# Optimization experiments

Measured on AMD Instinct MI355X. Metric: run time of the kernel, lower is better.

The kernel has to match this reference:

```python
import jax, jax.numpy as jnp
import numpy as np

NUM_JOINT_LIST = [8, 10, 12, 14, 16, 18, 20, 22, 24, 9, 13, 17]
NUM_GLOBAL_LIST = [1, 0, 1, 1, 0, 1, 1, 1, 0, 1, 1, 1]
M = len(NUM_JOINT_LIST)
B, T, JMAX = 16, 128, 24
H, HEADS, L, RANK = 256, 8, 4, 8
DH = H // HEADS
LAYERSCALE = 1e-4


def setup_inputs():
    key = jax.random.key(0)
    ks = jax.random.split(key, 40)
    m_idx = jax.random.randint(ks[0], (B,), 0, M)
    nj = jnp.array(NUM_JOINT_LIST)[m_idx]
    valid = jnp.arange(JMAX)[None, :] < nj[:, None]  # (B, J) real joints of each morphology
    jtype = jax.random.randint(ks[1], (B, JMAX), 0, 3)  # 0 slide, 1 hinge, 2 global
    has_g = (jnp.array(NUM_GLOBAL_LIST) > 0)[m_idx][:, None]
    jtype = jnp.where((jtype == 2) & ~has_g, 0, jtype)
    tile = lambda m: jnp.broadcast_to(m[:, None, :], (B, T, JMAX))
    slide_mask = tile((jtype == 0) & valid)
    hinge_mask = tile((jtype == 1) & valid)
    global_mask = tile((jtype == 2) & valid)
    act_mask = tile(valid)
    morph_mask = (valid[:, :, None] & valid[:, None, :]) | jnp.eye(JMAX, dtype=bool)[None]
    act = jax.random.normal(ks[2], (B, T, JMAX, 1), dtype=jnp.float32)
    s = 0.02
    inp = dict(act=act, slide_mask=slide_mask, hinge_mask=hinge_mask,
               global_mask=global_mask, act_mask=act_mask, morph_mask=morph_mask,
               m_idx=m_idx)
    inp['Ws'] = s * jax.random.normal(ks[3], (1, H)); inp['bs'] = jnp.zeros((H,))
    inp['Wh'] = s * jax.random.normal(ks[4], (1, H)); inp['bh'] = jnp.zeros((H,))
    inp['Wg'] = s * jax.random.normal(ks[5], (M, H))
    inp['Wact'] = s * jax.random.normal(ks[6], (1, H))
    pos = jax.random.normal(ks[7], (M, JMAX, H))
    pos_valid = jnp.arange(JMAX)[None, :, None] < jnp.array(NUM_JOINT_LIST)[:, None, None]
    inp['pos'] = pos * pos_valid  # rows beyond num_joint stay zero, as in the torch loop
    inp['ln1_s'] = jnp.ones((L, H)); inp['ln1_b'] = jnp.zeros((L, H))
    inp['Wqkv'] = s * jax.random.normal(ks[8], (L, H, 3 * H)); inp['bqkv'] = jnp.zeros((L, 3 * H))
    inp['loraA'] = s * jax.random.normal(ks[9], (L, M, H, RANK))
    inp['loraB'] = s * jax.random.normal(ks[10], (L, M, RANK, 3 * H))
    inp['Wo'] = s * jax.random.normal(ks[11], (L, H, H)); inp['bo'] = jnp.zeros((L, H))
    inp['ln2_s'] = jnp.ones((L, H)); inp['ln2_b'] = jnp.zeros((L, H))
    inp['W1'] = s * jax.random.normal(ks[12], (L, H, 4 * H)); inp['b1'] = jnp.zeros((L, 4 * H))
    inp['W2'] = s * jax.random.normal(ks[13], (L, 4 * H, H)); inp['b2'] = jnp.zeros((L, H))
    inp['g1'] = LAYERSCALE * jnp.ones((L, H)); inp['g2'] = LAYERSCALE * jnp.ones((L, H))
    inp['lnf_s'] = jnp.ones((H,)); inp['lnf_b'] = jnp.zeros((H,))
    return inp


def _ln(z, sc, bi):
    mu = z.mean(-1, keepdims=True)
    v = ((z - mu) ** 2).mean(-1, keepdims=True)
    return (z - mu) * jax.lax.rsqrt(v + 1e-5) * sc + bi


def reference(act, slide_mask, hinge_mask, global_mask, act_mask, morph_mask, m_idx,
              Ws, bs, Wh, bh, Wg, Wact, pos,
              ln1_s, ln1_b, Wqkv, bqkv, loraA, loraB, Wo, bo,
              ln2_s, ln2_b, W1, b1, W2, b2, g1, g2, lnf_s, lnf_b):
    has_g = (jnp.array(NUM_GLOBAL_LIST) > 0)[m_idx]  # (B,)
    a1 = act[..., :1]  # slide_dim = hinge_dim = num_global = 1
    emb = jnp.where(slide_mask[..., None], a1 @ Ws + bs, jnp.zeros((), act.dtype))
    emb = jnp.where(hinge_mask[..., None], a1 @ Wh + bh, emb)
    emb_g = a1 * Wg[m_idx][:, None, None, :]  # per-sample morphology-routed projection
    emb = jnp.where((global_mask & has_g[:, None, None])[..., None], emb_g, emb)
    y = emb + act_mask[..., None].astype(emb.dtype) * Wact[0]
    y = y + pos[m_idx][:, None]  # (B, T, J, H)
    Bv, Tv, J, _ = y.shape
    N = Bv * Tv
    x = y.reshape(N, J, H)
    amask = jnp.broadcast_to(morph_mask[:, None], (Bv, Tv, J, J)).reshape(N, J, J)
    t_idx = jnp.repeat(m_idx, Tv)  # (N,)
    neg = jnp.finfo(x.dtype).min
    scale = 1.0 / np.sqrt(DH)

    def block(x, lp):
        l1s, l1b, wqkv, bq, lA, lB, wo, bo_, l2s, l2b, w1, b1_, w2, b2_, gg1, gg2 = lp
        h = _ln(x, l1s, l1b)
        qkv = h @ wqkv + bq
        # per-task LoRA on qkv, gathered by morphology index
        qkv = qkv + jnp.einsum('njr,nrk->njk', jnp.einsum('njd,ndr->njr', h, lA[t_idx]), lB[t_idx])
        q, k, v = jnp.split(qkv, 3, axis=-1)
        q = q.reshape(N, J, HEADS, DH).transpose(0, 2, 1, 3)
        k = k.reshape(N, J, HEADS, DH).transpose(0, 2, 1, 3)
        v = v.reshape(N, J, HEADS, DH).transpose(0, 2, 1, 3)
        scores = jnp.einsum('nhid,nhjd->nhij', q, k) * scale
        scores = jnp.where(amask[:, None], scores, neg)
        attn = jax.nn.softmax(scores, axis=-1)
        o = jnp.einsum('nhij,nhjd->nhid', attn, v).transpose(0, 2, 1, 3).reshape(N, J, H)
        x = x + gg1 * (o @ wo + bo_)
        h2 = _ln(x, l2s, l2b)
        x = x + gg2 * (jax.nn.gelu(h2 @ w1 + b1_) @ w2 + b2_)
        return x, None

    x, _ = jax.lax.scan(block, x, (ln1_s, ln1_b, Wqkv, bqkv, loraA, loraB, Wo, bo,
                                   ln2_s, ln2_b, W1, b1, W2, b2, g1, g2))
    x = _ln(x, lnf_s, lnf_b)
    return x.reshape(Bv, Tv, J, H)
```

## Files before the change

kernel.cpp:

```cpp
#include <hip/hip_runtime.h>
#include <cstdint>
#include <cstddef>

#define B_     16
#define T_     128
#define J_     24
#define H_     256
#define HEADS_ 8
#define DH_    32
#define L_     4
#define RANK_  8
#define M_     12
#define NTOK   (B_*T_)
#define ROWS   (NTOK*J_)
#define KQ     320
#define HAS_G_MASK 3821

typedef __attribute__((ext_vector_type(8))) short short8;
typedef __attribute__((ext_vector_type(4))) float f32x4;

__constant__ int cNJ[M_] = {8, 10, 12, 14, 16, 18, 20, 22, 24, 9, 13, 17};

__device__ __forceinline__ float bf2f(unsigned short u) {
    union { unsigned int i; float f; } c; c.i = ((unsigned int)u) << 16; return c.f;
}
__device__ __forceinline__ unsigned short f2bf(float f) {
    union { float f; unsigned int i; } c; c.f = f;
    unsigned int x = c.i;
    return (unsigned short)((x + 0x7fffu + ((x >> 16) & 1u)) >> 16);
}
__device__ __forceinline__ float asf(unsigned int u) {
    union { unsigned int i; float f; } c; c.i = u; return c.f;
}
__device__ __forceinline__ unsigned int cvtpk(float lo, float hi) {
    unsigned int r;
    asm("v_cvt_pk_bf16_f32 %0, %1, %2" : "=v"(r) : "v"(lo), "v"(hi));
    return r;
}
__device__ __forceinline__ void gload16(const void* g, void* l) {
    __builtin_amdgcn_global_load_lds((const __attribute__((address_space(1))) void*)g,
                                     (__attribute__((address_space(3))) void*)l, 16, 0, 0);
}

__global__ void zero_flag(int* f) { *f = 0; }

__global__ __launch_bounds__(256) void detect_kernel(
    const unsigned char* __restrict__ sl, const unsigned char* __restrict__ hi,
    const unsigned char* __restrict__ gl, const int* __restrict__ m_idx,
    int* __restrict__ flag) {
    int rj = blockIdx.x * 256 + threadIdx.x;
    if (rj >= ROWS) return;
    int b = rj / (T_ * J_);
    int j = rj % J_;
    int valid = (j < cNJ[m_idx[b]]) ? 1 : 0;
    int cnt = (sl[rj] != 0) + (hi[rj] != 0) + (gl[rj] != 0);
    if (cnt != valid) atomicOr(flag, 1);
}

__global__ void wconv_t(const float* __restrict__ W, unsigned short* __restrict__ WT,
                        int K, int Nc, int total) {
    int i = blockIdx.x * 256 + threadIdx.x;
    if (i >= total) return;
    int kn = K * Nc;
    int l = i / kn;
    int r = i - l * kn;
    int n = r / K;
    int k = r - n * K;
    WT[i] = f2bf(W[(size_t)l * kn + (size_t)k * Nc + n]);
}

__global__ void wconv_qkv(const float* __restrict__ Wqkv, const float* __restrict__ loraB,
                          unsigned short* __restrict__ OT) {
    int i = blockIdx.x * 256 + threadIdx.x;
    const int total = L_ * M_ * 768 * KQ;
    if (i >= total) return;
    int k = i % KQ;
    int n = (i / KQ) % 768;
    int m = (i / (KQ * 768)) % M_;
    int l = i / (KQ * 768 * M_);
    float v = 0.f;
    if (k < 256)      v = Wqkv[((size_t)l * 256 + k) * 768 + n];
    else if (k < 264) v = loraB[(((size_t)l * M_ + m) * RANK_ + (k - 256)) * 768 + n];
    OT[i] = f2bf(v);
}

__global__ __launch_bounds__(256) void embed_kernel(
    const float* __restrict__ act, const void* __restrict__ slide,
    const void* __restrict__ hinge, const void* __restrict__ glob,
    const int* __restrict__ m_idx, const int* __restrict__ flag,
    const float* __restrict__ Ws, const float* __restrict__ bs,
    const float* __restrict__ Wh, const float* __restrict__ bh,
    const float* __restrict__ Wg, const float* __restrict__ Wact,
    const float* __restrict__ pos, float* __restrict__ X) {
    int rj = (blockIdx.x << 2) + (threadIdx.x >> 6);
    int lane = threadIdx.x & 63;
    int b = rj / (T_ * J_);
    int j = rj % J_;
    int m = m_idx[b];
    bool valid = j < cNJ[m];
    bool s, hh, gl;
    if (*flag) {
        s  = ((const int*)slide)[rj] != 0;
        hh = ((const int*)hinge)[rj] != 0;
        gl = ((const int*)glob)[rj]  != 0;
    } else {
        s  = ((const unsigned char*)slide)[rj] != 0;
        hh = ((const unsigned char*)hinge)[rj] != 0;
        gl = ((const unsigned char*)glob)[rj]  != 0;
    }
    float a1 = act[rj];
    int h0 = lane << 2;
    float e0 = 0.f, e1 = 0.f, e2 = 0.f, e3 = 0.f;
    if (s) {
        float4 w = *(const float4*)(Ws + h0); float4 bb = *(const float4*)(bs + h0);
        e0 = a1 * w.x + bb.x; e1 = a1 * w.y + bb.y; e2 = a1 * w.z + bb.z; e3 = a1 * w.w + bb.w;
    } else if (hh) {
        float4 w = *(const float4*)(Wh + h0); float4 bb = *(const float4*)(bh + h0);
        e0 = a1 * w.x + bb.x; e1 = a1 * w.y + bb.y; e2 = a1 * w.z + bb.z; e3 = a1 * w.w + bb.w;
    } else if (gl && ((HAS_G_MASK >> m) & 1)) {
        float4 w = *(const float4*)(Wg + m * H_ + h0);
        e0 = a1 * w.x; e1 = a1 * w.y; e2 = a1 * w.z; e3 = a1 * w.w;
    }
    if (valid) {
        float4 wa = *(const float4*)(Wact + h0);
        e0 += wa.x; e1 += wa.y; e2 += wa.z; e3 += wa.w;
    }
    float4 pv = *(const float4*)(pos + (size_t)(m * J_ + j) * H_ + h0);
    float4 out; out.x = e0 + pv.x; out.y = e1 + pv.y; out.z = e2 + pv.z; out.w = e3 + pv.w;
    *(float4*)(X + ((size_t)rj << 8) + h0) = out;
}

template<bool LORA>
__global__ __launch_bounds__(256) void ln_kernel(
    const float* __restrict__ X, const float* __restrict__ sc, const float* __restrict__ bi,
    const float* __restrict__ lA, const int* __restrict__ m_idx,
    unsigned short* __restrict__ Hbf, int ldh) {
    int row = (blockIdx.x << 2) + (threadIdx.x >> 6);
    int lane = threadIdx.x & 63;
    int h0 = lane << 2;
    float4 xv = *(const float4*)(X + ((size_t)row << 8) + h0);
    float s1 = xv.x + xv.y + xv.z + xv.w;
    float s2 = xv.x * xv.x + xv.y * xv.y + xv.z * xv.z + xv.w * xv.w;
    #pragma unroll
    for (int o = 32; o; o >>= 1) { s1 += __shfl_xor(s1, o); s2 += __shfl_xor(s2, o); }
    float mu = s1 * (1.f / H_);
    float var = s2 * (1.f / H_) - mu * mu;
    float rs = rsqrtf(var + 1e-5f);
    float4 scv = *(const float4*)(sc + h0);
    float4 biv = *(const float4*)(bi + h0);
    float hn0 = (xv.x - mu) * rs * scv.x + biv.x;
    float hn1 = (xv.y - mu) * rs * scv.y + biv.y;
    float hn2 = (xv.z - mu) * rs * scv.z + biv.z;
    float hn3 = (xv.w - mu) * rs * scv.w + biv.w;
    ushort4 o4; o4.x = f2bf(hn0); o4.y = f2bf(hn1); o4.z = f2bf(hn2); o4.w = f2bf(hn3);
    *(ushort4*)(Hbf + (size_t)row * ldh + h0) = o4;
    if (LORA) {
        int t = m_idx[row / (J_ * T_)];
        const float* Ap = lA + (size_t)t * (H_ * RANK_) + h0 * RANK_;
        float4 av[8];
        #pragma unroll
        for (int c = 0; c < 8; ++c) av[c] = ((const float4*)Ap)[c];
        float hn[4] = {hn0, hn1, hn2, hn3};
        float p[RANK_];
        #pragma unroll
        for (int k = 0; k < RANK_; ++k) p[k] = 0.f;
        #pragma unroll
        for (int i = 0; i < 4; ++i)
            #pragma unroll
            for (int k = 0; k < RANK_; ++k) {
                int idx = i * RANK_ + k;
                float a = (idx & 3) == 0 ? av[idx >> 2].x : (idx & 3) == 1 ? av[idx >> 2].y
                        : (idx & 3) == 2 ? av[idx >> 2].z : av[idx >> 2].w;
                p[k] += hn[i] * a;
            }
        #pragma unroll
        for (int k = 0; k < RANK_; ++k)
            #pragma unroll
            for (int o = 32; o; o >>= 1) p[k] += __shfl_xor(p[k], o);
        unsigned int w0 = (unsigned int)f2bf(p[0]) | ((unsigned int)f2bf(p[1]) << 16);
        unsigned int w1 = (unsigned int)f2bf(p[2]) | ((unsigned int)f2bf(p[3]) << 16);
        unsigned int w2 = (unsigned int)f2bf(p[4]) | ((unsigned int)f2bf(p[5]) << 16);
        unsigned int w3 = (unsigned int)f2bf(p[6]) | ((unsigned int)f2bf(p[7]) << 16);
        unsigned int tv = 0;
        if (lane == 0) tv = w0; else if (lane == 1) tv = w1;
        else if (lane == 2) tv = w2; else if (lane == 3) tv = w3;
        if (lane < 32)
            *((unsigned int*)(Hbf + (size_t)row * ldh + 256) + lane) = tv;
    }
}

__global__ __launch_bounds__(256) void lnf_kernel(
    float* __restrict__ X, const float* __restrict__ sc, const float* __restrict__ bi) {
    int row = (blockIdx.x << 2) + (threadIdx.x >> 6);
    int lane = threadIdx.x & 63;
    int h0 = lane << 2;
    float4 xv = *(const float4*)(X + ((size_t)row << 8) + h0);
    float s1 = xv.x + xv.y + xv.z + xv.w;
    float s2 = xv.x * xv.x + xv.y * xv.y + xv.z * xv.z + xv.w * xv.w;
    #pragma unroll
    for (int o = 32; o; o >>= 1) { s1 += __shfl_xor(s1, o); s2 += __shfl_xor(s2, o); }
    float mu = s1 * (1.f / H_);
    float var = s2 * (1.f / H_) - mu * mu;
    float rs = rsqrtf(var + 1e-5f);
    float4 scv = *(const float4*)(sc + h0);
    float4 biv = *(const float4*)(bi + h0);
    float4 out;
    out.x = (xv.x - mu) * rs * scv.x + biv.x;
    out.y = (xv.y - mu) * rs * scv.y + biv.y;
    out.z = (xv.z - mu) * rs * scv.z + biv.z;
    out.w = (xv.w - mu) * rs * scv.w + biv.w;
    *(float4*)(X + ((size_t)row << 8) + h0) = out;
}

template<int EPI>
__global__ __launch_bounds__(256) void gemm_k(
    const unsigned short* __restrict__ A, const unsigned short* __restrict__ BT,
    const float* __restrict__ bias,
    const float* __restrict__ aux1,
    const int* __restrict__ m_idx,
    unsigned short* __restrict__ outB, float* __restrict__ outF,
    int K, int Nc) {
    __shared__ __align__(16) unsigned short As[128 * 64];
    __shared__ __align__(16) unsigned short Bs[128 * 64];
    int gx = gridDim.x;
    int nwg = gx * gridDim.y;
    int id = blockIdx.y * gx + blockIdx.x;
    int bx = blockIdx.x, by = blockIdx.y;
    if ((nwg & 7) == 0) {
        int q8 = nwg >> 3;
        int sid = (id & 7) * q8 + (id >> 3);
        bx = sid % gx; by = sid / gx;
    }
    int col0 = bx * 128;
    int row0 = by * 128;
    int tid = threadIdx.x;
    int wv = tid >> 6, lane = tid & 63;
    int wm = wv >> 1, wn = wv & 1;

    if (EPI == 0) BT += (size_t)m_idx[row0 / (J_ * T_)] * (768 * KQ);

    f32x4 acc[4][4];
    const f32x4 z = {0.f, 0.f, 0.f, 0.f};
    #pragma unroll
    for (int mi = 0; mi < 4; ++mi)
        #pragma unroll
        for (int ni = 0; ni < 4; ++ni) acc[mi][ni] = z;

    for (int k0 = 0; k0 < K; k0 += 64) {
        #pragma unroll
        for (int it = 0; it < 4; ++it) {
            int f = (tid << 4) + (it << 12);
            int r = f >> 7;
            int ce = (f & 127) >> 1;
            gload16(A  + (size_t)(row0 + r) * K + k0 + ce, (char*)As + f);
            gload16(BT + (size_t)(col0 + r) * K + k0 + ce, (char*)Bs + f);
        }
        __syncthreads();
        #pragma unroll
        for (int kk = 0; kk < 64; kk += 32) {
            short8 af[4], bfr[4];
            int ko = kk + ((lane >> 4) << 3);
            #pragma unroll
            for (int q = 0; q < 4; ++q) {
                af[q]  = *(const short8*)(As + ((wm * 64 + q * 16 + (lane & 15)) << 6) + ko);
                bfr[q] = *(const short8*)(Bs + ((wn * 64 + q * 16 + (lane & 15)) << 6) + ko);
            }
            #pragma unroll
            for (int mi = 0; mi < 4; ++mi)
                #pragma unroll
                for (int ni = 0; ni < 4; ++ni)
                    acc[mi][ni] = __builtin_amdgcn_mfma_f32_16x16x32_bf16(af[mi], bfr[ni], acc[mi][ni], 0, 0, 0);
        }
        __syncthreads();
    }

    int rbase = row0 + wm * 64 + ((lane >> 4) << 2);
    int cbase = col0 + wn * 64 + (lane & 15);

    if (EPI == 0 || EPI == 1) {
        const int ld = (EPI == 0) ? 768 : Nc;
        bool oddl = (lane & 1);
        int colp = cbase - (oddl ? 1 : 0);
        #pragma unroll
        for (int ni = 0; ni < 4; ++ni) {
            float bv = bias[cbase + ni * 16];
            #pragma unroll
            for (int mi = 0; mi < 4; ++mi) {
                float v[4], y[4];
                #pragma unroll
                for (int r = 0; r < 4; ++r) {
                    float u = acc[mi][ni][r] + bv;
                    if (EPI == 1) {
                        float t = u * u;
                        float p = fmaf(t, 0.044715f, 1.0f) * u;
                        float e = __expf(-1.5957691216057308f * p);
                        u = u / (1.f + e);
                    }
                    v[r] = u;
                }
                #pragma unroll
                for (int r = 0; r < 4; ++r) y[r] = __shfl_xor(v[r], 1);
                float f0 = oddl ? y[2] : v[0];
                float s0 = oddl ? v[2] : y[0];
                float f1 = oddl ? y[3] : v[1];
                float s1 = oddl ? v[3] : y[1];
                unsigned int p0 = cvtpk(f0, s0);
                unsigned int p1 = cvtpk(f1, s1);
                int rr = rbase + mi * 16 + (oddl ? 2 : 0);
                *(unsigned int*)(outB + (size_t)rr * ld + colp + ni * 16) = p0;
                *(unsigned int*)(outB + (size_t)(rr + 1) * ld + colp + ni * 16) = p1;
            }
        }
    } else {
        #pragma unroll
        for (int mi = 0; mi < 4; ++mi)
            #pragma unroll
            for (int r = 0; r < 4; ++r) {
                int row = rbase + mi * 16 + r;
                #pragma unroll
                for (int ni = 0; ni < 4; ++ni) {
                    int col = cbase + ni * 16;
                    float u = acc[mi][ni][r] + bias[col];
                    outF[(size_t)row * H_ + col] += aux1[col] * u;
                }
            }
    }
}

__global__ __launch_bounds__(256) void attn_kernel(
    const unsigned short* __restrict__ QKV, const int* __restrict__ m_idx,
    unsigned short* __restrict__ O) {
    __shared__ unsigned int q2s[4][24][18];
    __shared__ unsigned int k2s[4][16][26];
    __shared__ unsigned int v2s[4][24][18];
    __shared__ float       scs[4][24][27];
    int w = threadIdx.x >> 6, lane = threadIdx.x & 63;
    int n = blockIdx.x >> 1;
    int hd = ((blockIdx.x & 1) << 2) + w;
    int nj = cNJ[m_idx[n >> 7]];
    unsigned int (*q2)[18] = q2s[w];
    unsigned int (*k2)[26] = k2s[w];
    unsigned int (*v2)[18] = v2s[w];
    float (*sc)[27] = scs[w];

    const unsigned short* base = QKV + (size_t)n * (J_ * 768) + hd * DH_;

    #pragma unroll
    for (int it = 0; it < 3; ++it) {
        int r = it * 64 + lane;
        int j = r >> 3, d0 = (r & 7) << 2, d2 = d0 >> 1;
        ushort4 x = *(const ushort4*)(base + (size_t)j * 768 + d0);
        q2[j][d2]     = (unsigned int)x.x | ((unsigned int)x.y << 16);
        q2[j][d2 + 1] = (unsigned int)x.z | ((unsigned int)x.w << 16);
    }
    #pragma unroll
    for (int it = 0; it < 3; ++it) {
        int r = it * 64 + lane;
        int j = r >> 3, d0 = (r & 7) << 2, d2 = d0 >> 1;
        ushort4 x = *(const ushort4*)(base + (size_t)j * 768 + 256 + d0);
        k2[d2][j]     = (unsigned int)x.x | ((unsigned int)x.y << 16);
        k2[d2 + 1][j] = (unsigned int)x.z | ((unsigned int)x.w << 16);
    }
    #pragma unroll
    for (int it = 0; it < 3; ++it) {
        int r = it * 64 + lane;
        int j = r >> 3, d0 = (r & 7) << 2, d2 = d0 >> 1;
        ushort4 x = *(const ushort4*)(base + (size_t)j * 768 + 512 + d0);
        v2[j][d2]     = (unsigned int)x.x | ((unsigned int)x.y << 16);
        v2[j][d2 + 1] = (unsigned int)x.z | ((unsigned int)x.w << 16);
    }

    int i = lane >> 1, half = lane & 1;
    if (lane < 48) {
        float qf[32];
        #pragma unroll
        for (int d2 = 0; d2 < 16; ++d2) {
            unsigned int x = q2[i][d2];
            qf[2 * d2]     = asf(x << 16);
            qf[2 * d2 + 1] = asf(x & 0xffff0000u);
        }
        int jb = half * 12;
        float s[12];
        #pragma unroll
        for (int jj = 0; jj < 12; ++jj) {
            int j = jb + jj;
            float acc = 0.f;
            #pragma unroll
            for (int d2 = 0; d2 < 16; ++d2) {
                unsigned int x = k2[d2][j];
                acc += qf[2 * d2] * asf(x << 16);
                acc += qf[2 * d2 + 1] * asf(x & 0xffff0000u);
            }
            bool ok = (i < nj && j < nj) || (i == j);
            s[jj] = ok ? acc * 0.17677669529663687f : -1e30f;
        }
        float mx = s[0];
        #pragma unroll
        for (int jj = 1; jj < 12; ++jj) mx = fmaxf(mx, s[jj]);
        mx = fmaxf(mx, __shfl_xor(mx, 1));
        float sm = 0.f;
        #pragma unroll
        for (int jj = 0; jj < 12; ++jj) { float e = __expf(s[jj] - mx); s[jj] = e; sm += e; }
        sm += __shfl_xor(sm, 1);
        float inv = 1.f / sm;
        #pragma unroll
        for (int jj = 0; jj < 12; ++jj) sc[i][jb + jj] = s[jj] * inv;
    }

    #pragma unroll
    for (int it = 0; it < 6; ++it) {
        int i2 = it * 4 + (lane >> 4), d2 = lane & 15;
        float olo = 0.f, ohi = 0.f;
        #pragma unroll
        for (int j = 0; j < J_; ++j) {
            float p = sc[i2][j];
            unsigned int x = v2[j][d2];
            olo += p * asf(x << 16);
            ohi += p * asf(x & 0xffff0000u);
        }
        unsigned int o = (unsigned int)f2bf(olo) | ((unsigned int)f2bf(ohi) << 16);
        *(unsigned int*)(O + (size_t)(n * J_ + i2) * H_ + hd * DH_ + 2 * d2) = o;
    }
}

extern "C" void kernel_launch(void* const* d_in, const int* in_sizes, int n_in,
                              void* d_out, int out_size, void* d_ws, size_t ws_size,
                              hipStream_t stream) {
    (void)in_sizes; (void)n_in; (void)out_size; (void)ws_size;
    const float* act   = (const float*)d_in[0];
    const void*  slide = d_in[1];
    const void*  hinge = d_in[2];
    const void*  glob  = d_in[3];
    const int* m_idx  = (const int*)d_in[6];
    const float* Ws   = (const float*)d_in[7];
    const float* bs   = (const float*)d_in[8];
    const float* Wh   = (const float*)d_in[9];
    const float* bh   = (const float*)d_in[10];
    const float* Wg   = (const float*)d_in[11];
    const float* Wact = (const float*)d_in[12];
    const float* pos  = (const float*)d_in[13];
    const float* ln1s = (const float*)d_in[14];
    const float* ln1b = (const float*)d_in[15];
    const float* Wqkv = (const float*)d_in[16];
    const float* bqkv = (const float*)d_in[17];
    const float* loraA= (const float*)d_in[18];
    const float* loraB= (const float*)d_in[19];
    const float* Wo   = (const float*)d_in[20];
    const float* bo   = (const float*)d_in[21];
    const float* ln2s = (const float*)d_in[22];
    const float* ln2b = (const float*)d_in[23];
    const float* W1   = (const float*)d_in[24];
    const float* b1   = (const float*)d_in[25];
    const float* W2   = (const float*)d_in[26];
    const float* b2   = (const float*)d_in[27];
    const float* g1   = (const float*)d_in[28];
    const float* g2   = (const float*)d_in[29];
    const float* lnfs = (const float*)d_in[30];
    const float* lnfb = (const float*)d_in[31];

    float* X = (float*)d_out;

    size_t off = 0;
    char* ws = (char*)d_ws;
    auto nxt = [&](size_t bytes) -> char* {
        char* p = ws + off; off += (bytes + 255) & ~(size_t)255; return p;
    };
    int*            dflag  = (int*)nxt(256);
    unsigned short* Hbf    = (unsigned short*)nxt((size_t)ROWS * KQ * 2);
    unsigned short* QKVG   = (unsigned short*)nxt((size_t)ROWS * 1024 * 2);
    unsigned short* WqkvTp = (unsigned short*)nxt((size_t)L_ * M_ * 768 * KQ * 2);
    unsigned short* WoT    = (unsigned short*)nxt((size_t)L_ * H_ * H_ * 2);
    unsigned short* W1T    = (unsigned short*)nxt((size_t)L_ * H_ * 1024 * 2);
    unsigned short* W2T    = (unsigned short*)nxt((size_t)L_ * 1024 * H_ * 2);
    unsigned short* Obf    = Hbf;

    zero_flag<<<1, 1, 0, stream>>>(dflag);
    detect_kernel<<<(ROWS + 255) / 256, 256, 0, stream>>>(
        (const unsigned char*)slide, (const unsigned char*)hinge,
        (const unsigned char*)glob, m_idx, dflag);

    wconv_qkv<<<(L_ * M_ * 768 * KQ + 255) / 256, 256, 0, stream>>>(Wqkv, loraB, WqkvTp);
    wconv_t<<<(L_ * H_ * H_   + 255) / 256, 256, 0, stream>>>(Wo, WoT, H_, H_,   L_ * H_ * H_);
    wconv_t<<<(L_ * H_ * 1024 + 255) / 256, 256, 0, stream>>>(W1, W1T, H_, 1024, L_ * H_ * 1024);
    wconv_t<<<(L_ * 1024 * H_ + 255) / 256, 256, 0, stream>>>(W2, W2T, 1024, H_, L_ * 1024 * H_);

    embed_kernel<<<ROWS / 4, 256, 0, stream>>>(act, slide, hinge, glob, m_idx, dflag,
                                               Ws, bs, Wh, bh, Wg, Wact, pos, X);

    for (int l = 0; l < L_; ++l) {
        ln_kernel<true><<<ROWS / 4, 256, 0, stream>>>(X, ln1s + l * H_, ln1b + l * H_,
                                                      loraA + (size_t)l * M_ * H_ * RANK_, m_idx, Hbf, KQ);
        gemm_k<0><<<dim3(6, 384), 256, 0, stream>>>(Hbf, WqkvTp + (size_t)l * M_ * 768 * KQ,
                                                    bqkv + l * 768, nullptr, m_idx,
                                                    QKVG, nullptr, KQ, 768);
        attn_kernel<<<NTOK * 2, 256, 0, stream>>>(QKVG, m_idx, Obf);
        gemm_k<2><<<dim3(2, 384), 256, 0, stream>>>(Obf, WoT + (size_t)l * H_ * H_,
                                                    bo + l * H_, g1 + l * H_, nullptr,
                                                    nullptr, X, H_, H_);
        ln_kernel<false><<<ROWS / 4, 256, 0, stream>>>(X, ln2s + l * H_, ln2b + l * H_,
                                                       nullptr, nullptr, Hbf, H_);
        gemm_k<1><<<dim3(8, 384), 256, 0, stream>>>(Hbf, W1T + (size_t)l * H_ * 1024,
                                                    b1 + l * 1024, nullptr, nullptr,
                                                    QKVG, nullptr, H_, 1024);
        gemm_k<2><<<dim3(2, 384), 256, 0, stream>>>(QKVG, W2T + (size_t)l * 1024 * H_,
                                                    b2 + l * H_, g2 + l * H_, nullptr,
                                                    nullptr, X, 1024, H_);
    }

    lnf_kernel<<<ROWS / 4, 256, 0, stream>>>(X, lnfs, lnfb);
}
```

Measured before the change: 1.449 ms.

## Double-buffer GEMM LDS tiles with XOR swizzle and per-element bf16 epilogue stores

```diff
diff --git a/kernel.cpp b/kernel.cpp
--- a/kernel.cpp
+++ b/kernel.cpp
@@ -32,15 +32,11 @@
 __device__ __forceinline__ float asf(unsigned int u) {
     union { unsigned int i; float f; } c; c.i = u; return c.f;
 }
-__device__ __forceinline__ unsigned int cvtpk(float lo, float hi) {
-    unsigned int r;
-    asm("v_cvt_pk_bf16_f32 %0, %1, %2" : "=v"(r) : "v"(lo), "v"(hi));
-    return r;
-}
 __device__ __forceinline__ void gload16(const void* g, void* l) {
     __builtin_amdgcn_global_load_lds((const __attribute__((address_space(1))) void*)g,
                                      (__attribute__((address_space(3))) void*)l, 16, 0, 0);
 }
+#define SWZ(r) ((((r) >> 1) & 3) << 4)
 
 __global__ void zero_flag(int* f) { *f = 0; }
 
@@ -220,8 +216,8 @@
     const int* __restrict__ m_idx,
     unsigned short* __restrict__ outB, float* __restrict__ outF,
     int K, int Nc) {
-    __shared__ __align__(16) unsigned short As[128 * 64];
-    __shared__ __align__(16) unsigned short Bs[128 * 64];
+    __shared__ __align__(16) char LA[2][8192];
+    __shared__ __align__(16) char LB[2][8192];
     int gx = gridDim.x;
     int nwg = gx * gridDim.y;
     int id = blockIdx.y * gx + blockIdx.x;
@@ -239,6 +235,21 @@
 
     if (EPI == 0) BT += (size_t)m_idx[row0 / (J_ * T_)] * (768 * KQ);
 
+    int srow  = tid >> 2;
+    int sbyte = (tid & 3) << 4;
+    int sce   = (sbyte ^ SWZ(srow)) >> 1;
+    const unsigned short* Ab = A  + (size_t)(row0 + srow) * K + sce;
+    const unsigned short* Bb = BT + (size_t)(col0 + srow) * K + sce;
+    char* la0 = &LA[0][0] + tid * 16;
+    char* lb0 = &LB[0][0] + tid * 16;
+    size_t rstep = (size_t)64 * K;
+
+    int ko2   = (lane >> 4) << 4;
+    int rswz  = SWZ(lane & 15);
+    int rdoff = ko2 ^ rswz;
+    int rowA0 = wm * 64 + (lane & 15);
+    int rowB0 = wn * 64 + (lane & 15);
+
     f32x4 acc[4][4];
     const f32x4 z = {0.f, 0.f, 0.f, 0.f};
     #pragma unroll
@@ -246,32 +257,47 @@
         #pragma unroll
         for (int ni = 0; ni < 4; ++ni) acc[mi][ni] = z;
 
-    for (int k0 = 0; k0 < K; k0 += 64) {
-        #pragma unroll
-        for (int it = 0; it < 4; ++it) {
-            int f = (tid << 4) + (it << 12);
-            int r = f >> 7;
-            int ce = (f & 127) >> 1;
-            gload16(A  + (size_t)(row0 + r) * K + k0 + ce, (char*)As + f);
-            gload16(BT + (size_t)(col0 + r) * K + k0 + ce, (char*)Bs + f);
+    const int nt = K >> 5;
+
+    gload16(Ab,             la0);
+    gload16(Ab + rstep,     la0 + 4096);
+    gload16(Bb,             lb0);
+    gload16(Bb + rstep,     lb0 + 4096);
+
+    int cur = 0;
+    for (int t = 0; t < nt; ++t) {
+        int k0n = (t + 1) << 5;
+        if (t + 1 < nt) {
+            char* lan = &LA[cur ^ 1][0] + tid * 16;
+            char* lbn = &LB[cur ^ 1][0] + tid * 16;
+            gload16(Ab + k0n,         lan);
+            gload16(Ab + rstep + k0n, lan + 4096);
+            gload16(Bb + k0n,         lbn);
+            gload16(Bb + rstep + k0n, lbn + 4096);
+            asm volatile("s_waitcnt vmcnt(4)" ::: "memory");
+        } else {
+            asm volatile("s_waitcnt vmcnt(0)" ::: "memory");
         }
-        __syncthreads();
-        #pragma unroll
-        for (int kk = 0; kk < 64; kk += 32) {
-            short8 af[4], bfr[4];
-            int ko = kk + ((lane >> 4) << 3);
+        __builtin_amdgcn_s_barrier();
+        __builtin_amdgcn_sched_barrier(0);
+
+        const char* pa = &LA[cur][0];
+        const char* pb = &LB[cur][0];
+        short8 af[4], bfr[4];
+        #pragma unroll
+        for (int q = 0; q < 4; ++q) {
+            af[q]  = *(const short8*)(pa + (rowA0 + q * 16) * 64 + rdoff);
+            bfr[q] = *(const short8*)(pb + (rowB0 + q * 16) * 64 + rdoff);
+        }
+        #pragma unroll
+        for (int mi = 0; mi < 4; ++mi)
             #pragma unroll
-            for (int q = 0; q < 4; ++q) {
-                af[q]  = *(const short8*)(As + ((wm * 64 + q * 16 + (lane & 15)) << 6) + ko);
-                bfr[q] = *(const short8*)(Bs + ((wn * 64 + q * 16 + (lane & 15)) << 6) + ko);
-            }
-            #pragma unroll
-            for (int mi = 0; mi < 4; ++mi)
-                #pragma unroll
-                for (int ni = 0; ni < 4; ++ni)
-                    acc[mi][ni] = __builtin_amdgcn_mfma_f32_16x16x32_bf16(af[mi], bfr[ni], acc[mi][ni], 0, 0, 0);
-        }
-        __syncthreads();
+            for (int ni = 0; ni < 4; ++ni)
+                acc[mi][ni] = __builtin_amdgcn_mfma_f32_16x16x32_bf16(af[mi], bfr[ni], acc[mi][ni], 0, 0, 0);
+
+        __builtin_amdgcn_sched_barrier(0);
+        __builtin_amdgcn_s_barrier();
+        cur ^= 1;
     }
 
     int rbase = row0 + wm * 64 + ((lane >> 4) << 2);
@@ -279,37 +305,22 @@
 
     if (EPI == 0 || EPI == 1) {
         const int ld = (EPI == 0) ? 768 : Nc;
-        bool oddl = (lane & 1);
-        int colp = cbase - (oddl ? 1 : 0);
         #pragma unroll
         for (int ni = 0; ni < 4; ++ni) {
             float bv = bias[cbase + ni * 16];
             #pragma unroll
-            for (int mi = 0; mi < 4; ++mi) {
-                float v[4], y[4];
+            for (int mi = 0; mi < 4; ++mi)
                 #pragma unroll
                 for (int r = 0; r < 4; ++r) {
                     float u = acc[mi][ni][r] + bv;
                     if (EPI == 1) {
-                        float t = u * u;
-                        float p = fmaf(t, 0.044715f, 1.0f) * u;
-                        float e = __expf(-1.5957691216057308f * p);
+                        float tt = u * u;
+                        float pp = fmaf(tt, 0.044715f, 1.0f) * u;
+                        float e = __expf(-1.5957691216057308f * pp);
                         u = u / (1.f + e);
                     }
-                    v[r] = u;
+                    outB[(size_t)(rbase + mi * 16 + r) * ld + cbase + ni * 16] = f2bf(u);
                 }
-                #pragma unroll
-                for (int r = 0; r < 4; ++r) y[r] = __shfl_xor(v[r], 1);
-                float f0 = oddl ? y[2] : v[0];
-                float s0 = oddl ? v[2] : y[0];
-                float f1 = oddl ? y[3] : v[1];
-                float s1 = oddl ? v[3] : y[1];
-                unsigned int p0 = cvtpk(f0, s0);
-                unsigned int p1 = cvtpk(f1, s1);
-                int rr = rbase + mi * 16 + (oddl ? 2 : 0);
-                *(unsigned int*)(outB + (size_t)rr * ld + colp + ni * 16) = p0;
-                *(unsigned int*)(outB + (size_t)(rr + 1) * ld + colp + ni * 16) = p1;
-            }
         }
     } else {
         #pragma unroll
@@ -495,15 +506,15 @@
                                                     QKVG, nullptr, KQ, 768);
         attn_kernel<<<NTOK * 2, 256, 0, stream>>>(QKVG, m_idx, Obf);
         gemm_k<2><<<dim3(2, 384), 256, 0, stream>>>(Obf, WoT + (size_t)l * H_ * H_,
-                                                    bo + l * H_, g1 + l * H_, nullptr,
+                                                    bo + l * H_, g1 + l * H_, m_idx,
                                                     nullptr, X, H_, H_);
         ln_kernel<false><<<ROWS / 4, 256, 0, stream>>>(X, ln2s + l * H_, ln2b + l * H_,
                                                        nullptr, nullptr, Hbf, H_);
         gemm_k<1><<<dim3(8, 384), 256, 0, stream>>>(Hbf, W1T + (size_t)l * H_ * 1024,
-                                                    b1 + l * 1024, nullptr, nullptr,
+                                                    b1 + l * 1024, nullptr, m_idx,
                                                     QKVG, nullptr, H_, 1024);
         gemm_k<2><<<dim3(2, 384), 256, 0, stream>>>(QKVG, W2T + (size_t)l * 1024 * H_,
-                                                    b2 + l * H_, g2 + l * H_, nullptr,
+                                                    b2 + l * H_, g2 + l * H_, m_idx,
                                                     nullptr, X, 1024, H_);
     }
 
```

New measurement: 1.317 ms. -9.1%, faster.
